# Optimization experiments

Measured on AMD Instinct MI355X. Metric: run time of the kernel, lower is better.

Reference implementation:

```python
import jax, jax.numpy as jnp
import numpy as np

METRIC_SCALE = 0.01  # metric = I + 0.01 * outer(p, p)


def setup_inputs() -> dict:
    key = jax.random.key(0)
    kq, kk = jax.random.split(key)
    query_points = jax.random.normal(kq, (8192, 512), dtype=jnp.float32)
    key_points = jax.random.normal(kk, (8192, 512), dtype=jnp.float32)
    return {"query_points": query_points, "key_points": key_points}


def reference(query_points, key_points):
    # diff_ij = q_i - k_j;  dist^2 under metric (I + c * p p^T) is
    # ||diff||^2 + c * (p . diff)^2 -- avoids materializing [Nq, Nk, d] diffs.
    c = METRIC_SCALE
    qq = jnp.sum(query_points * query_points, axis=-1)          # [Nq]
    kk = jnp.sum(key_points * key_points, axis=-1)              # [Nk]
    qk = jnp.einsum('qd,kd->qk', query_points, key_points)      # [Nq, Nk]
    norm2 = jnp.maximum(qq[:, None] + kk[None, :] - 2.0 * qk, 0.0)
    qdot = qq[:, None] - qk                                     # q_i . (q_i - k_j)
    kdot = qk - kk[None, :]                                     # k_j . (q_i - k_j) (sign irrelevant, squared)
    query_dist = jnp.sqrt(norm2 + c * qdot * qdot)
    key_dist = jnp.sqrt(norm2 + c * kdot * kdot)
    scores = -0.5 * (query_dist + key_dist)
    return jax.nn.softmax(scores, axis=-1)
```

## Files before the change

### kernel.cpp

```cpp
#include <hip/hip_runtime.h>
#include <stdint.h>


#define NQ 8192
#define NK 8192
#define DIM 512
#define CSCALE 0.01f

typedef float f32x4 __attribute__((ext_vector_type(4)));
typedef short s16x8 __attribute__((ext_vector_type(8)));
typedef unsigned short u16x4 __attribute__((ext_vector_type(4)));

__device__ __forceinline__ unsigned short f2bf(float x) {
  union { float f; uint32_t u; } c; c.f = x;
  uint32_t u = c.u;
  return (unsigned short)((u + 0x7fffu + ((u >> 16) & 1u)) >> 16);
}

__device__ __forceinline__ float bf2f(unsigned short h) {
  union { uint32_t u; float f; } c; c.u = ((uint32_t)h) << 16;
  return c.f;
}

__device__ __forceinline__ s16x8 pack8(f32x4 a, f32x4 b) {
  s16x8 r;
  r[0]=(short)f2bf(a.x); r[1]=(short)f2bf(a.y);
  r[2]=(short)f2bf(a.z); r[3]=(short)f2bf(a.w);
  r[4]=(short)f2bf(b.x); r[5]=(short)f2bf(b.y);
  r[6]=(short)f2bf(b.z); r[7]=(short)f2bf(b.w);
  return r;
}

#define GLOAD_LDS16(g, l)                                                      \
  __builtin_amdgcn_global_load_lds(                                            \
      (const __attribute__((address_space(1))) void*)(g),                      \
      (__attribute__((address_space(3))) void*)(l), 16, 0, 0)

__global__ __launch_bounds__(256) void prep_full_kernel(
    const float* __restrict__ q, const float* __restrict__ k,
    unsigned short* __restrict__ qbf, unsigned short* __restrict__ kbf,
    float* __restrict__ qq, float* __restrict__ kk) {
  int rowg = blockIdx.x * 4 + (threadIdx.x >> 6);
  int lane = threadIdx.x & 63;
  const float* src; unsigned short* dst; float* nrm; int row;
  if (rowg < NQ) { src = q; dst = qbf; nrm = qq; row = rowg; }
  else           { src = k; dst = kbf; nrm = kk; row = rowg - NQ; }
  const float* p = src + (size_t)row * DIM + lane * 8;
  f32x4 a = *(const f32x4*)p;
  f32x4 b = *(const f32x4*)(p + 4);
  float ss = a.x*a.x + a.y*a.y + a.z*a.z + a.w*a.w
           + b.x*b.x + b.y*b.y + b.z*b.z + b.w*b.w;
  *(s16x8*)(dst + (size_t)row * DIM + lane * 8) = pack8(a, b);
#pragma unroll
  for (int mask = 1; mask < 64; mask <<= 1) ss += __shfl_xor(ss, mask, 64);
  if (lane == 0) nrm[row] = ss;
}

__global__ __launch_bounds__(256) void prep_norms_kernel(
    const float* __restrict__ q, const float* __restrict__ k,
    float* __restrict__ qq, float* __restrict__ kk) {
  int rowg = blockIdx.x * 4 + (threadIdx.x >> 6);
  int lane = threadIdx.x & 63;
  const float* src; float* nrm; int row;
  if (rowg < NQ) { src = q; nrm = qq; row = rowg; }
  else           { src = k; nrm = kk; row = rowg - NQ; }
  const float* p = src + (size_t)row * DIM + lane * 8;
  f32x4 a = *(const f32x4*)p;
  f32x4 b = *(const f32x4*)(p + 4);
  float ss = a.x*a.x + a.y*a.y + a.z*a.z + a.w*a.w
           + b.x*b.x + b.y*b.y + b.z*b.z + b.w*b.w;
#pragma unroll
  for (int mask = 1; mask < 64; mask <<= 1) ss += __shfl_xor(ss, mask, 64);
  if (lane == 0) nrm[row] = ss;
}

__device__ __forceinline__ float score_fn(float qkv, float qqv, float kkv) {
  float n2 = fmaxf(qqv + kkv - 2.f * qkv, 0.f);
  float qd = qqv - qkv;
  float kd = qkv - kkv;
  return -0.5f * (__builtin_amdgcn_sqrtf(n2 + CSCALE * qd * qd) +
                  __builtin_amdgcn_sqrtf(n2 + CSCALE * kd * kd));
}

__global__ __launch_bounds__(256) void gemm_exp_kernel(
    const unsigned short* __restrict__ qbf, const unsigned short* __restrict__ kbf,
    const float* __restrict__ qq, const float* __restrict__ kk,
    unsigned short* __restrict__ E) {
  __shared__ alignas(16) unsigned short smem[16384];
  const int tid = threadIdx.x;
  const int m0 = blockIdx.y * 128;
  const int n0 = blockIdx.x * 128;
  const int wave = tid >> 6, lane = tid & 63;
  const int wr = wave >> 1, wc = wave & 1;
  const int quad = lane >> 4, lcol = lane & 15;

  const int srow = tid >> 2;
  const int gsw = (tid & 3) ^ ((srow >> 1) & 3);
  const unsigned short* ga = qbf + (size_t)(m0 + srow) * DIM + gsw * 8;
  const unsigned short* gb = kbf + (size_t)(n0 + srow) * DIM + gsw * 8;
  char* labase = (char*)smem;
  const int stageoff = wave * 1024;

  f32x4 acc[4][4];
#pragma unroll
  for (int mi = 0; mi < 4; ++mi)
#pragma unroll
    for (int ni = 0; ni < 4; ++ni) acc[mi][ni] = f32x4{0.f, 0.f, 0.f, 0.f};

  const int arow = wr * 64 + lcol;
  const int brow = wc * 64 + lcol;
  const int swz = (lcol >> 1) & 3;
  const int qsw = quad ^ swz;

#define STAGE_TILE(bufbyte, ko)                                                \
  do {                                                                         \
    GLOAD_LDS16(ga + (ko), labase + (bufbyte) + stageoff);                     \
    GLOAD_LDS16(ga + (ko) + 64 * DIM, labase + (bufbyte) + stageoff + 4096);   \
    GLOAD_LDS16(gb + (ko), labase + (bufbyte) + 8192 + stageoff);              \
    GLOAD_LDS16(gb + (ko) + 64 * DIM,                                          \
                labase + (bufbyte) + 8192 + stageoff + 4096);                  \
  } while (0)

#define COMPUTE_TILE(bufbyte)                                                  \
  do {                                                                         \
    const s16x8* lA8 = (const s16x8*)(labase + (bufbyte));                     \
    const s16x8* lB8 = (const s16x8*)(labase + (bufbyte) + 8192);              \
    s16x8 af[4], bfr[4];                                                       \
    _Pragma("unroll")                                                          \
    for (int mi = 0; mi < 4; ++mi) af[mi] = lA8[(arow + mi * 16) * 4 + qsw];   \
    _Pragma("unroll")                                                          \
    for (int ni = 0; ni < 4; ++ni) bfr[ni] = lB8[(brow + ni * 16) * 4 + qsw];  \
    _Pragma("unroll")                                                          \
    for (int mi = 0; mi < 4; ++mi)                                             \
      _Pragma("unroll")                                                        \
      for (int ni = 0; ni < 4; ++ni)                                           \
        acc[mi][ni] = __builtin_amdgcn_mfma_f32_16x16x32_bf16(                 \
            af[mi], bfr[ni], acc[mi][ni], 0, 0, 0);                            \
  } while (0)

#define SYNC_PIPE()                                                            \
  do {                                                                         \
    asm volatile("s_waitcnt vmcnt(0)" ::: "memory");                           \
    __builtin_amdgcn_s_barrier();                                              \
  } while (0)

  const int NT = DIM / 32;
  STAGE_TILE(0, 0);
  SYNC_PIPE();
#pragma unroll 1
  for (int kt = 0; kt < NT; kt += 2) {
    STAGE_TILE(16384, (kt + 1) * 32);
    COMPUTE_TILE(0);
    SYNC_PIPE();
    if (kt + 2 < NT) STAGE_TILE(0, (kt + 2) * 32);
    COMPUTE_TILE(16384);
    SYNC_PIPE();
  }
#undef STAGE_TILE
#undef COMPUTE_TILE
#undef SYNC_PIPE

  unsigned short* tw = smem + wave * 1280;
  float kkv[4];
#pragma unroll
  for (int ni = 0; ni < 4; ++ni) kkv[ni] = kk[n0 + wc * 64 + ni * 16 + lcol];
#pragma unroll
  for (int mi = 0; mi < 4; ++mi) {
    const int ibase = m0 + wr * 64 + mi * 16 + quad * 4;
    float qqv[4];
#pragma unroll
    for (int r = 0; r < 4; ++r) qqv[r] = qq[ibase + r];
#pragma unroll
    for (int ni = 0; ni < 4; ++ni)
#pragma unroll
      for (int r = 0; r < 4; ++r) {
        float e = __expf(score_fn(acc[mi][ni][r], qqv[r], kkv[ni]));
        tw[(quad * 4 + r) * 80 + ((ni ^ quad) * 16 + lcol)] = f2bf(e);
      }
#pragma unroll
    for (int j = 0; j < 2; ++j) {
      const int row16 = (lane >> 3) + j * 8;
      const int g = (lane & 7) >> 1;
      const int off = row16 * 80 + ((g ^ (row16 >> 2)) * 16) + (lane & 1) * 8;
      s16x8 vv = *(const s16x8*)(tw + off);
      const int rowg = m0 + wr * 64 + mi * 16 + row16;
      *(s16x8*)(E + (size_t)rowg * NK + n0 + wc * 64 + (lane & 7) * 8) = vv;
    }
  }
}

__global__ __launch_bounds__(256) void rowsum_scale_kernel(
    const unsigned short* __restrict__ E, float* __restrict__ out) {
  __shared__ float red[4];
  const int t = threadIdx.x;
  const int wave = t >> 6, lane = t & 63;
  const unsigned short* Erow = E + (size_t)blockIdx.x * NK;
  float* Orow = out + (size_t)blockIdx.x * NK;
  s16x8 ev[4];
  float s = 0.f;
#pragma unroll
  for (int j = 0; j < 4; ++j) {
    ev[j] = *(const s16x8*)(Erow + j * 2048 + t * 8);
    float a0 = bf2f((unsigned short)ev[j][0]) + bf2f((unsigned short)ev[j][1]);
    float a1 = bf2f((unsigned short)ev[j][2]) + bf2f((unsigned short)ev[j][3]);
    float a2 = bf2f((unsigned short)ev[j][4]) + bf2f((unsigned short)ev[j][5]);
    float a3 = bf2f((unsigned short)ev[j][6]) + bf2f((unsigned short)ev[j][7]);
    s += (a0 + a1) + (a2 + a3);
  }
#pragma unroll
  for (int mask = 1; mask < 64; mask <<= 1) s += __shfl_xor(s, mask, 64);
  if (lane == 0) red[wave] = s;
  __syncthreads();
  float z = 1.0f / ((red[0] + red[1]) + (red[2] + red[3]));
#pragma unroll
  for (int j = 0; j < 4; ++j) {
    f32x4 lo, hi;
    lo.x = bf2f((unsigned short)ev[j][0]) * z;
    lo.y = bf2f((unsigned short)ev[j][1]) * z;
    lo.z = bf2f((unsigned short)ev[j][2]) * z;
    lo.w = bf2f((unsigned short)ev[j][3]) * z;
    hi.x = bf2f((unsigned short)ev[j][4]) * z;
    hi.y = bf2f((unsigned short)ev[j][5]) * z;
    hi.z = bf2f((unsigned short)ev[j][6]) * z;
    hi.w = bf2f((unsigned short)ev[j][7]) * z;
    *(f32x4*)(Orow + j * 2048 + t * 8) = lo;
    *(f32x4*)(Orow + j * 2048 + t * 8 + 4) = hi;
  }
}

__device__ __forceinline__ void score_epilogue(
    const f32x4 acc[4][4], const float* __restrict__ qq,
    const float* __restrict__ kk, float* __restrict__ S,
    int m0, int n0, int wr, int wc, int quad, int lcol) {
  float kkv[4];
#pragma unroll
  for (int ni = 0; ni < 4; ++ni) kkv[ni] = kk[n0 + wc * 64 + ni * 16 + lcol];
#pragma unroll
  for (int mi = 0; mi < 4; ++mi) {
    const int ibase = m0 + wr * 64 + mi * 16 + quad * 4;
    float qqv[4];
#pragma unroll
    for (int r = 0; r < 4; ++r) qqv[r] = qq[ibase + r];
#pragma unroll
    for (int ni = 0; ni < 4; ++ni) {
      const int col = n0 + wc * 64 + ni * 16 + lcol;
#pragma unroll
      for (int r = 0; r < 4; ++r)
        S[(size_t)(ibase + r) * NK + col] = score_fn(acc[mi][ni][r], qqv[r], kkv[ni]);
    }
  }
}

__global__ __launch_bounds__(256) void gemm_fast_kernel(
    const unsigned short* __restrict__ qbf, const unsigned short* __restrict__ kbf,
    const float* __restrict__ qq, const float* __restrict__ kk,
    float* __restrict__ S) {
  __shared__ unsigned short lA[128 * 32];
  __shared__ unsigned short lB[128 * 32];
  const int tid = threadIdx.x;
  const int m0 = blockIdx.y * 128;
  const int n0 = blockIdx.x * 128;
  const int wave = tid >> 6, lane = tid & 63;
  const int wr = wave >> 1, wc = wave & 1;
  const int quad = lane >> 4, lcol = lane & 15;
  const unsigned short* ga = qbf + (size_t)(m0 + (tid >> 2)) * DIM + (tid & 3) * 8;
  const unsigned short* gb = kbf + (size_t)(n0 + (tid >> 2)) * DIM + (tid & 3) * 8;
  char* la0 = (char*)lA + wave * 1024;
  char* lb0 = (char*)lB + wave * 1024;
  f32x4 acc[4][4];
#pragma unroll
  for (int mi = 0; mi < 4; ++mi)
#pragma unroll
    for (int ni = 0; ni < 4; ++ni) acc[mi][ni] = f32x4{0.f, 0.f, 0.f, 0.f};
  const s16x8* lA8 = (const s16x8*)lA;
  const s16x8* lB8 = (const s16x8*)lB;
  const int arow = wr * 64 + lcol;
  const int brow = wc * 64 + lcol;
  for (int kt = 0; kt < DIM / 32; ++kt) {
    const int ko = kt * 32;
    GLOAD_LDS16(ga + ko, la0);
    GLOAD_LDS16(ga + ko + 64 * DIM, la0 + 4096);
    GLOAD_LDS16(gb + ko, lb0);
    GLOAD_LDS16(gb + ko + 64 * DIM, lb0 + 4096);
    __syncthreads();
    s16x8 af[4], bfr[4];
#pragma unroll
    for (int mi = 0; mi < 4; ++mi) af[mi] = lA8[(arow + mi * 16) * 4 + quad];
#pragma unroll
    for (int ni = 0; ni < 4; ++ni) bfr[ni] = lB8[(brow + ni * 16) * 4 + quad];
#pragma unroll
    for (int mi = 0; mi < 4; ++mi)
#pragma unroll
      for (int ni = 0; ni < 4; ++ni)
        acc[mi][ni] = __builtin_amdgcn_mfma_f32_16x16x32_bf16(
            af[mi], bfr[ni], acc[mi][ni], 0, 0, 0);
    __syncthreads();
  }
  score_epilogue(acc, qq, kk, S, m0, n0, wr, wc, quad, lcol);
}

__global__ __launch_bounds__(256) void gemm_safe_kernel(
    const float* __restrict__ q, const float* __restrict__ k,
    const float* __restrict__ qq, const float* __restrict__ kk,
    float* __restrict__ S) {
  __shared__ unsigned short lA[128 * 32];
  __shared__ unsigned short lB[128 * 32];
  const int tid = threadIdx.x;
  const int m0 = blockIdx.y * 128;
  const int n0 = blockIdx.x * 128;
  const int wave = tid >> 6, lane = tid & 63;
  const int wr = wave >> 1, wc = wave & 1;
  const int quad = lane >> 4, lcol = lane & 15;
  const float* gaf = q + (size_t)(m0 + (tid >> 1)) * DIM + (tid & 1) * 16;
  const float* gbf = k + (size_t)(n0 + (tid >> 1)) * DIM + (tid & 1) * 16;
  unsigned short* wA = lA + (tid >> 1) * 32 + (tid & 1) * 16;
  unsigned short* wB = lB + (tid >> 1) * 32 + (tid & 1) * 16;
  f32x4 acc[4][4];
#pragma unroll
  for (int mi = 0; mi < 4; ++mi)
#pragma unroll
    for (int ni = 0; ni < 4; ++ni) acc[mi][ni] = f32x4{0.f, 0.f, 0.f, 0.f};
  const s16x8* lA8 = (const s16x8*)lA;
  const s16x8* lB8 = (const s16x8*)lB;
  const int arow = wr * 64 + lcol;
  const int brow = wc * 64 + lcol;
  for (int kt = 0; kt < DIM / 32; ++kt) {
    const float* pa = gaf + kt * 32;
    const float* pb = gbf + kt * 32;
    f32x4 a0 = *(const f32x4*)(pa), a1 = *(const f32x4*)(pa + 4);
    f32x4 a2 = *(const f32x4*)(pa + 8), a3 = *(const f32x4*)(pa + 12);
    f32x4 b0 = *(const f32x4*)(pb), b1 = *(const f32x4*)(pb + 4);
    f32x4 b2 = *(const f32x4*)(pb + 8), b3 = *(const f32x4*)(pb + 12);
    *(s16x8*)wA = pack8(a0, a1);
    *(s16x8*)(wA + 8) = pack8(a2, a3);
    *(s16x8*)wB = pack8(b0, b1);
    *(s16x8*)(wB + 8) = pack8(b2, b3);
    __syncthreads();
    s16x8 af[4], bfr[4];
#pragma unroll
    for (int mi = 0; mi < 4; ++mi) af[mi] = lA8[(arow + mi * 16) * 4 + quad];
#pragma unroll
    for (int ni = 0; ni < 4; ++ni) bfr[ni] = lB8[(brow + ni * 16) * 4 + quad];
#pragma unroll
    for (int mi = 0; mi < 4; ++mi)
#pragma unroll
      for (int ni = 0; ni < 4; ++ni)
        acc[mi][ni] = __builtin_amdgcn_mfma_f32_16x16x32_bf16(
            af[mi], bfr[ni], acc[mi][ni], 0, 0, 0);
    __syncthreads();
  }
  score_epilogue(acc, qq, kk, S, m0, n0, wr, wc, quad, lcol);
}

__global__ __launch_bounds__(256) void rowsoftmax_kernel(float* __restrict__ S) {
  __shared__ float red[8];
  const int t = threadIdx.x;
  const int wave = t >> 6, lane = t & 63;
  float* Srow = S + (size_t)blockIdx.x * NK;
  f32x4 v[8];
  float m = -1e30f;
#pragma unroll
  for (int j = 0; j < 8; ++j) {
    v[j] = *(const f32x4*)(Srow + j * 1024 + t * 4);
    m = fmaxf(m, fmaxf(fmaxf(v[j].x, v[j].y), fmaxf(v[j].z, v[j].w)));
  }
#pragma unroll
  for (int mask = 1; mask < 64; mask <<= 1) m = fmaxf(m, __shfl_xor(m, mask, 64));
  if (lane == 0) red[wave] = m;
  __syncthreads();
  m = fmaxf(fmaxf(red[0], red[1]), fmaxf(red[2], red[3]));
  float s = 0.f;
#pragma unroll
  for (int j = 0; j < 8; ++j) {
    v[j].x = __expf(v[j].x - m);
    v[j].y = __expf(v[j].y - m);
    v[j].z = __expf(v[j].z - m);
    v[j].w = __expf(v[j].w - m);
    s += (v[j].x + v[j].y) + (v[j].z + v[j].w);
  }
#pragma unroll
  for (int mask = 1; mask < 64; mask <<= 1) s += __shfl_xor(s, mask, 64);
  if (lane == 0) red[4 + wave] = s;
  __syncthreads();
  float z = 1.0f / ((red[4] + red[5]) + (red[6] + red[7]));
#pragma unroll
  for (int j = 0; j < 8; ++j) {
    v[j].x *= z; v[j].y *= z; v[j].z *= z; v[j].w *= z;
    *(f32x4*)(Srow + j * 1024 + t * 4) = v[j];
  }
}

extern "C" void kernel_launch(void* const* d_in, const int* in_sizes, int n_in,
                              void* d_out, int out_size, void* d_ws, size_t ws_size,
                              hipStream_t stream) {
  const float* q = (const float*)d_in[0];
  const float* k = (const float*)d_in[1];
  float* S = (float*)d_out;
  char* ws = (char*)d_ws;

  if (ws_size >= (size_t)151126016) {
    unsigned short* qbf = (unsigned short*)(ws);
    unsigned short* kbf = (unsigned short*)(ws + 8388608);
    float* qq = (float*)(ws + 16777216);
    float* kk = (float*)(ws + 16777216 + 32768);
    unsigned short* E = (unsigned short*)(ws + 16908288);
    prep_full_kernel<<<4096, 256, 0, stream>>>(q, k, qbf, kbf, qq, kk);
    gemm_exp_kernel<<<dim3(64, 64), 256, 0, stream>>>(qbf, kbf, qq, kk, E);
    rowsum_scale_kernel<<<NQ, 256, 0, stream>>>(E, S);
  } else if (ws_size >= (size_t)16842752) {
    unsigned short* qbf = (unsigned short*)(ws);
    unsigned short* kbf = (unsigned short*)(ws + 8388608);
    float* qq = (float*)(ws + 16777216);
    float* kk = (float*)(ws + 16777216 + 32768);
    prep_full_kernel<<<4096, 256, 0, stream>>>(q, k, qbf, kbf, qq, kk);
    gemm_fast_kernel<<<dim3(64, 64), 256, 0, stream>>>(qbf, kbf, qq, kk, S);
    rowsoftmax_kernel<<<NQ, 256, 0, stream>>>(S);
  } else {
    float* qq = (float*)(ws);
    float* kk = (float*)(ws + 32768);
    prep_norms_kernel<<<4096, 256, 0, stream>>>(q, k, qq, kk);
    gemm_safe_kernel<<<dim3(64, 64), 256, 0, stream>>>(q, k, qq, kk, S);
    rowsoftmax_kernel<<<NQ, 256, 0, stream>>>(S);
  }
}
```

Measured before the change: 432.1 us.

## Enlarge GEMM tile to 256x256 with triple-buffered LDS pipeline and block swizzle

The bf16 GEMM+exp kernel moves from 128x128 tiles with 4 waves to 256x256 tiles with 8 waves. Each wave now holds 8x4 MFMA accumulators, and LDS grows to three stages with a vmcnt(4) wait so loads run two k-steps ahead. Block indices are remapped to group tiles for L2 reuse, and s_setprio wraps the MFMA bursts. Each tile is reused more from global memory, at the cost of more registers, more LDS, and only 1024 blocks to spread across the CUs.

```diff
diff --git a/kernel.cpp b/kernel.cpp
--- a/kernel.cpp
+++ b/kernel.cpp
@@ -82,91 +82,104 @@
                   __builtin_amdgcn_sqrtf(n2 + CSCALE * kd * kd));
 }
 
-__global__ __launch_bounds__(256) void gemm_exp_kernel(
+__global__ __launch_bounds__(512, 2) void gemm_exp256_kernel(
     const unsigned short* __restrict__ qbf, const unsigned short* __restrict__ kbf,
     const float* __restrict__ qq, const float* __restrict__ kk,
     unsigned short* __restrict__ E) {
-  __shared__ alignas(16) unsigned short smem[16384];
+  __shared__ alignas(16) unsigned short smem[49152];
   const int tid = threadIdx.x;
-  const int m0 = blockIdx.y * 128;
-  const int n0 = blockIdx.x * 128;
+  const int lin = blockIdx.y * 32 + blockIdx.x;
+  const int tile = (lin & 7) * 128 + (lin >> 3);
+  const int m0 = (tile >> 5) * 256;
+  const int n0 = (tile & 31) * 256;
   const int wave = tid >> 6, lane = tid & 63;
-  const int wr = wave >> 1, wc = wave & 1;
+  const int wrM = wave >> 2, wcN = wave & 3;
   const int quad = lane >> 4, lcol = lane & 15;
 
   const int srow = tid >> 2;
-  const int gsw = (tid & 3) ^ ((srow >> 1) & 3);
-  const unsigned short* ga = qbf + (size_t)(m0 + srow) * DIM + gsw * 8;
-  const unsigned short* gb = kbf + (size_t)(n0 + srow) * DIM + gsw * 8;
-  char* labase = (char*)smem;
-  const int stageoff = wave * 1024;
-
-  f32x4 acc[4][4];
-#pragma unroll
-  for (int mi = 0; mi < 4; ++mi)
+  const int kkey = (srow ^ (srow >> 2)) & 3;
+  const int gsw = (tid & 3) ^ kkey;
+  const unsigned short* gaA = qbf + (size_t)(m0 + srow) * DIM + gsw * 8;
+  const unsigned short* gbB = kbf + (size_t)(n0 + srow) * DIM + gsw * 8;
+  char* sm8 = (char*)smem;
+  const int wso = wave * 1024;
+
+#define STAGE_A(b, kt)                                                         \
+  do {                                                                         \
+    GLOAD_LDS16(gaA + (kt) * 32, sm8 + (b) * 32768 + wso);                     \
+    GLOAD_LDS16(gaA + (kt) * 32 + 128 * DIM, sm8 + (b) * 32768 + 8192 + wso);  \
+  } while (0)
+#define STAGE_B(b, kt)                                                         \
+  do {                                                                         \
+    GLOAD_LDS16(gbB + (kt) * 32, sm8 + (b) * 32768 + 16384 + wso);             \
+    GLOAD_LDS16(gbB + (kt) * 32 + 128 * DIM,                                   \
+                sm8 + (b) * 32768 + 16384 + 8192 + wso);                       \
+  } while (0)
+
+  f32x4 acc[8][4];
+#pragma unroll
+  for (int mi = 0; mi < 8; ++mi)
 #pragma unroll
     for (int ni = 0; ni < 4; ++ni) acc[mi][ni] = f32x4{0.f, 0.f, 0.f, 0.f};
 
-  const int arow = wr * 64 + lcol;
-  const int brow = wc * 64 + lcol;
-  const int swz = (lcol >> 1) & 3;
-  const int qsw = quad ^ swz;
-
-#define STAGE_TILE(bufbyte, ko)                                                \
-  do {                                                                         \
-    GLOAD_LDS16(ga + (ko), labase + (bufbyte) + stageoff);                     \
-    GLOAD_LDS16(ga + (ko) + 64 * DIM, labase + (bufbyte) + stageoff + 4096);   \
-    GLOAD_LDS16(gb + (ko), labase + (bufbyte) + 8192 + stageoff);              \
-    GLOAD_LDS16(gb + (ko) + 64 * DIM,                                          \
-                labase + (bufbyte) + 8192 + stageoff + 4096);                  \
-  } while (0)
-
-#define COMPUTE_TILE(bufbyte)                                                  \
-  do {                                                                         \
-    const s16x8* lA8 = (const s16x8*)(labase + (bufbyte));                     \
-    const s16x8* lB8 = (const s16x8*)(labase + (bufbyte) + 8192);              \
-    s16x8 af[4], bfr[4];                                                       \
-    _Pragma("unroll")                                                          \
-    for (int mi = 0; mi < 4; ++mi) af[mi] = lA8[(arow + mi * 16) * 4 + qsw];   \
-    _Pragma("unroll")                                                          \
-    for (int ni = 0; ni < 4; ++ni) bfr[ni] = lB8[(brow + ni * 16) * 4 + qsw];  \
-    _Pragma("unroll")                                                          \
-    for (int mi = 0; mi < 4; ++mi)                                             \
-      _Pragma("unroll")                                                        \
-      for (int ni = 0; ni < 4; ++ni)                                           \
-        acc[mi][ni] = __builtin_amdgcn_mfma_f32_16x16x32_bf16(                 \
-            af[mi], bfr[ni], acc[mi][ni], 0, 0, 0);                            \
-  } while (0)
-
-#define SYNC_PIPE()                                                            \
-  do {                                                                         \
-    asm volatile("s_waitcnt vmcnt(0)" ::: "memory");                           \
-    __builtin_amdgcn_s_barrier();                                              \
-  } while (0)
-
-  const int NT = DIM / 32;
-  STAGE_TILE(0, 0);
-  SYNC_PIPE();
+  const s16x8* L8 = (const s16x8*)smem;
+  const int slot = quad ^ ((lcol ^ (lcol >> 2)) & 3);
+  const int arow = wrM * 128 + lcol;
+  const int brow = wcN * 64 + lcol;
+
+  STAGE_A(0, 0); STAGE_B(0, 0);
+  STAGE_A(1, 1); STAGE_B(1, 1);
+  asm volatile("s_waitcnt vmcnt(4)" ::: "memory");
+  __builtin_amdgcn_s_barrier();
+
+  int cur = 0, stg = 2;
 #pragma unroll 1
-  for (int kt = 0; kt < NT; kt += 2) {
-    STAGE_TILE(16384, (kt + 1) * 32);
-    COMPUTE_TILE(0);
-    SYNC_PIPE();
-    if (kt + 2 < NT) STAGE_TILE(0, (kt + 2) * 32);
-    COMPUTE_TILE(16384);
-    SYNC_PIPE();
-  }
-#undef STAGE_TILE
-#undef COMPUTE_TILE
-#undef SYNC_PIPE
+  for (int kt = 0; kt < 16; ++kt) {
+    const int bb = cur * 2048;
+    s16x8 bfr[4], af[4];
+#pragma unroll
+    for (int ni = 0; ni < 4; ++ni)
+      bfr[ni] = L8[bb + 1024 + (brow + ni * 16) * 4 + slot];
+#pragma unroll
+    for (int mi = 0; mi < 4; ++mi)
+      af[mi] = L8[bb + (arow + mi * 16) * 4 + slot];
+    if (kt <= 13) STAGE_A(stg, kt + 2);
+    __builtin_amdgcn_s_setprio(1);
+#pragma unroll
+    for (int mi = 0; mi < 4; ++mi)
+#pragma unroll
+      for (int ni = 0; ni < 4; ++ni)
+        acc[mi][ni] = __builtin_amdgcn_mfma_f32_16x16x32_bf16(
+            af[mi], bfr[ni], acc[mi][ni], 0, 0, 0);
+    __builtin_amdgcn_s_setprio(0);
+#pragma unroll
+    for (int mi = 0; mi < 4; ++mi)
+      af[mi] = L8[bb + (arow + 64 + mi * 16) * 4 + slot];
+    if (kt <= 13) STAGE_B(stg, kt + 2);
+    __builtin_amdgcn_s_setprio(1);
+#pragma unroll
+    for (int mi = 0; mi < 4; ++mi)
+#pragma unroll
+      for (int ni = 0; ni < 4; ++ni)
+        acc[4 + mi][ni] = __builtin_amdgcn_mfma_f32_16x16x32_bf16(
+            af[mi], bfr[ni], acc[4 + mi][ni], 0, 0, 0);
+    __builtin_amdgcn_s_setprio(0);
+    if (kt <= 13)      asm volatile("s_waitcnt vmcnt(4)" ::: "memory");
+    else               asm volatile("s_waitcnt vmcnt(0)" ::: "memory");
+    __builtin_amdgcn_s_barrier();
+    cur = (cur == 2) ? 0 : cur + 1;
+    stg = (stg == 2) ? 0 : stg + 1;
+  }
+#undef STAGE_A
+#undef STAGE_B
 
   unsigned short* tw = smem + wave * 1280;
   float kkv[4];
 #pragma unroll
-  for (int ni = 0; ni < 4; ++ni) kkv[ni] = kk[n0 + wc * 64 + ni * 16 + lcol];
-#pragma unroll
-  for (int mi = 0; mi < 4; ++mi) {
-    const int ibase = m0 + wr * 64 + mi * 16 + quad * 4;
+  for (int ni = 0; ni < 4; ++ni) kkv[ni] = kk[n0 + wcN * 64 + ni * 16 + lcol];
+#pragma unroll
+  for (int mi = 0; mi < 8; ++mi) {
+    const int ibase = m0 + wrM * 128 + mi * 16 + quad * 4;
     float qqv[4];
 #pragma unroll
     for (int r = 0; r < 4; ++r) qqv[r] = qq[ibase + r];
@@ -183,8 +196,8 @@
       const int g = (lane & 7) >> 1;
       const int off = row16 * 80 + ((g ^ (row16 >> 2)) * 16) + (lane & 1) * 8;
       s16x8 vv = *(const s16x8*)(tw + off);
-      const int rowg = m0 + wr * 64 + mi * 16 + row16;
-      *(s16x8*)(E + (size_t)rowg * NK + n0 + wc * 64 + (lane & 7) * 8) = vv;
+      const int rowg = m0 + wrM * 128 + mi * 16 + row16;
+      *(s16x8*)(E + (size_t)rowg * NK + n0 + wcN * 64 + (lane & 7) * 8) = vv;
     }
   }
 }
@@ -405,7 +418,7 @@
     float* kk = (float*)(ws + 16777216 + 32768);
     unsigned short* E = (unsigned short*)(ws + 16908288);
     prep_full_kernel<<<4096, 256, 0, stream>>>(q, k, qbf, kbf, qq, kk);
-    gemm_exp_kernel<<<dim3(64, 64), 256, 0, stream>>>(qbf, kbf, qq, kk, E);
+    gemm_exp256_kernel<<<dim3(32, 32), 512, 0, stream>>>(qbf, kbf, qq, kk, E);
     rowsum_scale_kernel<<<NQ, 256, 0, stream>>>(E, S);
   } else if (ws_size >= (size_t)16842752) {
     unsigned short* qbf = (unsigned short*)(ws);
```

After: 418.9 us. 3.0% less time.
